# Performance work log

Hardware: AMD Instinct MI355X
Metric: run time of the kernel (lower is better)

The kernel has to match this reference:

```python
import jax, jax.numpy as jnp
import numpy as np

EPS = 1e-4
HEADS = 16
DH = 64


def setup_inputs() -> dict:
    key = jax.random.key(0)
    ks = jax.random.split(key, 5)
    b, t, d = 2, 2048, 1024
    return {
        "X": jax.random.normal(ks[0], (b, t, d), dtype=jnp.float32),
        "W_in": jax.random.normal(ks[1], (HEADS * 4 * DH, d), dtype=jnp.float32) * (1.0 / np.sqrt(d)),
        "b_in": jax.random.normal(ks[2], (HEADS * 4 * DH,), dtype=jnp.float32) * 0.01,
        "W_out": jax.random.normal(ks[3], (d, HEADS * DH), dtype=jnp.float32) * (1.0 / np.sqrt(HEADS * DH)),
        "b_out": jax.random.normal(ks[4], (d,), dtype=jnp.float32) * 0.01,
    }


def reference(X, W_in, b_in, W_out, b_out):
    b, t, d = X.shape
    # project_in: [b,t,h*4*dh] -> [b,t,h,4*dh] -> [b,h,t,4*dh]
    P = jnp.einsum('btd,ed->bte', X, W_in) + b_in
    P = P.reshape(b, t, HEADS, 4 * DH).transpose(0, 2, 1, 3)
    Q, K, V, G = jnp.split(P, 4, axis=-1)  # each [b,h,t,dh]
    # Euclidean cdist: sqrt(||q||^2 + ||k||^2 - 2 q.k), clamped at 0
    q2 = jnp.sum(Q * Q, axis=-1)[..., :, None]   # [b,h,t,1]
    k2 = jnp.sum(K * K, axis=-1)[..., None, :]   # [b,h,1,t]
    qk = jnp.einsum('bhqd,bhkd->bhqk', Q, K)
    dist = jnp.sqrt(jnp.maximum(q2 + k2 - 2.0 * qk, 0.0))
    # Shepard weights: (eps + dist)^-2, normalized over keys
    W = (EPS + dist) ** (-2)
    W = W / (EPS + jnp.sum(W, axis=-1, keepdims=True))
    A = jnp.einsum('bhqk,bhkd->bhqd', W, V)
    # gate, merge heads: [b,h,t,dh] -> [b,t,h*dh]
    H = (G * A).transpose(0, 2, 1, 3).reshape(b, t, HEADS * DH)
    Y = jnp.einsum('bte,de->btd', H, W_out) + b_out
    return Y
```

## Files before the change

### kernel.cpp

```cpp
#include <hip/hip_runtime.h>
#include <math.h>

#define EPS 1e-4f


typedef __attribute__((ext_vector_type(8))) short bf16x8;
typedef __attribute__((ext_vector_type(4))) float f32x4;

#define MFMA(a, b, c) __builtin_amdgcn_mfma_f32_16x16x32_bf16(a, b, c, 0, 0, 0)

__device__ __forceinline__ unsigned short f2b(float f) {
    unsigned int u = __float_as_uint(f);
    u += 0x7fffu + ((u >> 16) & 1u);
    return (unsigned short)(u >> 16);
}
__device__ __forceinline__ float b2f(unsigned short u) {
    return __uint_as_float(((unsigned int)u) << 16);
}
__device__ __forceinline__ unsigned int cvtpk(float a, float b) {
    unsigned int r;
    asm("v_cvt_pk_bf16_f32 %0, %1, %2" : "=v"(r) : "v"(a), "v"(b));
    return r;
}

__global__ __launch_bounds__(256)
void sga_f2b(const float* __restrict__ src, unsigned short* __restrict__ dst, int n8) {
    int i = blockIdx.x * 256 + threadIdx.x;
    const int stride = gridDim.x * 256;
    for (; i < n8; i += stride) {
        const float4* s = (const float4*)src + i * 2;
        float4 a = s[0], b = s[1];
        uint4 o;
        o.x = (unsigned)f2b(a.x) | ((unsigned)f2b(a.y) << 16);
        o.y = (unsigned)f2b(a.z) | ((unsigned)f2b(a.w) << 16);
        o.z = (unsigned)f2b(b.x) | ((unsigned)f2b(b.y) << 16);
        o.w = (unsigned)f2b(b.z) | ((unsigned)f2b(b.w) << 16);
        *((uint4*)dst + i) = o;
    }
}

__global__ __launch_bounds__(256)
void sga_gemm1(const unsigned short* __restrict__ Xb, const unsigned short* __restrict__ Wb,
               const float* __restrict__ bin,
               unsigned short* __restrict__ Qb, unsigned short* __restrict__ Kb,
               unsigned short* __restrict__ Vt, unsigned short* __restrict__ Gb)
{
    __shared__ unsigned short As[128 * 40];
    __shared__ unsigned short Bs[128 * 40];
    const int tid = threadIdx.x;
    const int lane = tid & 63, w = tid >> 6;
    const int lr = lane & 15, lg = lane >> 4;
    const int wm = w & 1, wn = w >> 1;
    const int m0 = blockIdx.y * 128, n0 = blockIdx.x * 128;
    const int r0 = tid >> 2, c0 = tid & 3;

    const unsigned short* Ap = Xb + (m0 + r0) * 1024 + c0 * 8;
    const unsigned short* Bp = Wb + (n0 + r0) * 1024 + c0 * 8;
    bf16x8 pa0 = *(const bf16x8*)Ap;
    bf16x8 pa1 = *(const bf16x8*)(Ap + 64 * 1024);
    bf16x8 pb0 = *(const bf16x8*)Bp;
    bf16x8 pb1 = *(const bf16x8*)(Bp + 64 * 1024);
    unsigned short* Aw = &As[r0 * 40 + c0 * 8];
    unsigned short* Bw = &Bs[r0 * 40 + c0 * 8];

    f32x4 acc[4][4] = {};

    for (int kt = 0; kt < 32; ++kt) {
        __syncthreads();
        *(bf16x8*)Aw = pa0; *(bf16x8*)(Aw + 64 * 40) = pa1;
        *(bf16x8*)Bw = pb0; *(bf16x8*)(Bw + 64 * 40) = pb1;
        __syncthreads();
        if (kt < 31) {
            Ap += 32; Bp += 32;
            pa0 = *(const bf16x8*)Ap; pa1 = *(const bf16x8*)(Ap + 64 * 1024);
            pb0 = *(const bf16x8*)Bp; pb1 = *(const bf16x8*)(Bp + 64 * 1024);
        }
        bf16x8 af[4], bfr[4];
        #pragma unroll
        for (int i = 0; i < 4; ++i)
            af[i] = *(const bf16x8*)&As[(wm * 64 + i * 16 + lr) * 40 + lg * 8];
        #pragma unroll
        for (int i = 0; i < 4; ++i)
            bfr[i] = *(const bf16x8*)&Bs[(wn * 64 + i * 16 + lr) * 40 + lg * 8];
        #pragma unroll
        for (int mi = 0; mi < 4; ++mi)
            #pragma unroll
            for (int ni = 0; ni < 4; ++ni)
                acc[mi][ni] = MFMA(af[mi], bfr[ni], acc[mi][ni]);
    }

    const int bb = m0 >> 11;
    #pragma unroll
    for (int mf = 0; mf < 4; ++mf) {
        const int tbase = m0 + wm * 64 + mf * 16 + lg * 4;
        const int tloc = tbase & 2047;
        #pragma unroll
        for (int nf = 0; nf < 4; ++nf) {
            const int n = n0 + wn * 64 + nf * 16 + lr;
            const int h = n >> 8, cc = n & 255;
            const int part = cc >> 6, j = cc & 63;
            const int bh = bb * 16 + h;
            const float bz = bin[n];
            f32x4 v = acc[mf][nf];
            unsigned short e0 = f2b(v[0] + bz), e1 = f2b(v[1] + bz),
                           e2 = f2b(v[2] + bz), e3 = f2b(v[3] + bz);
            if (part == 2) {
                ushort4 pk = make_ushort4(e0, e1, e2, e3);
                *(ushort4*)&Vt[(bh * 64 + j) * 2048 + tloc] = pk;
            } else {
                unsigned short* dst = (part == 0) ? Qb : ((part == 1) ? Kb : Gb);
                unsigned short vv[4] = {e0, e1, e2, e3};
                #pragma unroll
                for (int r = 0; r < 4; ++r)
                    dst[(bh * 2048 + tloc + r) * 64 + j] = vv[r];
            }
        }
    }
}

__global__ __launch_bounds__(256)
void sga_norms(const unsigned short* __restrict__ Qb, const unsigned short* __restrict__ Kb,
               float* __restrict__ q2s, float* __restrict__ k2s)
{
    const int idx = blockIdx.x * 256 + threadIdx.x;
    const unsigned short* q = Qb + idx * 64;
    const unsigned short* k = Kb + idx * 64;
    float sq = 0.f, sk = 0.f;
    #pragma unroll
    for (int c = 0; c < 8; ++c) {
        bf16x8 a = *(const bf16x8*)(q + c * 8);
        bf16x8 b = *(const bf16x8*)(k + c * 8);
        #pragma unroll
        for (int e = 0; e < 8; ++e) {
            float f = b2f((unsigned short)a[e]); sq += f * f;
            float g = b2f((unsigned short)b[e]); sk += g * g;
        }
    }
    q2s[idx] = sq;
    k2s[idx] = sk;
}

__global__ __launch_bounds__(256, 3)
void sga_attn(const unsigned short* __restrict__ Qb, const unsigned short* __restrict__ Kb,
              const unsigned short* __restrict__ Vt,
              const float* __restrict__ q2s, const float* __restrict__ k2s,
              unsigned short* __restrict__ Op0, unsigned short* __restrict__ Op1,
              unsigned short* __restrict__ Op2,
              float* __restrict__ Sw0, float* __restrict__ Sw1, float* __restrict__ Sw2)
{
    __shared__ unsigned short Klds[2 * 4096];
    __shared__ unsigned short Vlds[2 * 4096];
    __shared__ unsigned short Wlds[4 * 2048];

    const int tid = threadIdx.x;
    const int lane = tid & 63, w = tid >> 6;
    const int lr = lane & 15, lg = lane >> 4;

    const int qt = blockIdx.x, bh = blockIdx.y, half = blockIdx.z;
    const int q0 = qt * 128 + w * 32;
    const int kbeg = half * 11;
    const int kend = (half == 2) ? 32 : (kbeg + 11);

    unsigned short* wl = &Wlds[w * 2048];
    unsigned short* __restrict__ Op = (half == 0) ? Op0 : ((half == 1) ? Op1 : Op2);
    float* __restrict__ Sw = (half == 0) ? Sw0 : ((half == 1) ? Sw1 : Sw2);

    const int srow = w * 16 + (lane >> 2);
    const int sc = (lane & 3) * 2;
    const unsigned short* Kg = Kb + (bh * 2048 + srow) * 64 + sc * 8;
    const unsigned short* Vg = Vt + (bh * 64 + srow) * 2048 + sc * 8;
    const int swz0 = srow * 64 + ((sc ^ (srow & 7)) * 8);
    const int swz1 = srow * 64 + (((sc + 1) ^ (srow & 7)) * 8);

    bf16x8 qf[2][2];
    #pragma unroll
    for (int g = 0; g < 2; ++g) {
        const unsigned short* qp = Qb + (bh * 2048 + q0 + g * 16 + lr) * 64 + lg * 8;
        qf[g][0] = *(const bf16x8*)qp;
        qf[g][1] = *(const bf16x8*)(qp + 32);
    }
    float q2v[2];
    q2v[0] = q2s[bh * 2048 + q0 + lr];
    q2v[1] = q2s[bh * 2048 + q0 + 16 + lr];

    f32x4 oacc[2][4] = {};
    float sumw[2] = {0.f, 0.f};

    uint4 ks0, ks1, vs0, vs1;
    {
        const unsigned short* kp = Kg + kbeg * 4096;
        ks0 = *(const uint4*)kp; ks1 = *(const uint4*)(kp + 8);
        const unsigned short* vp = Vg + kbeg * 64;
        vs0 = *(const uint4*)vp; vs1 = *(const uint4*)(vp + 8);
    }
    *(uint4*)&Klds[swz0] = ks0; *(uint4*)&Klds[swz1] = ks1;
    *(uint4*)&Vlds[swz0] = vs0; *(uint4*)&Vlds[swz1] = vs1;
    __syncthreads();

    int buf = 0;
    for (int kt = kbeg; kt < kend; ++kt) {
        const int k0 = kt * 64;
        const bool more = (kt + 1 < kend);

        if (more) {
            const unsigned short* kp = Kg + (kt + 1) * 4096;
            ks0 = *(const uint4*)kp; ks1 = *(const uint4*)(kp + 8);
            const unsigned short* vp = Vg + (kt + 1) * 64;
            vs0 = *(const uint4*)vp; vs1 = *(const uint4*)(vp + 8);
        }

        f32x4 k2v[4];
        #pragma unroll
        for (int nf = 0; nf < 4; ++nf)
            k2v[nf] = *(const f32x4*)&k2s[bh * 2048 + k0 + nf * 16 + lg * 4];

        f32x4 sa[2][4] = {};
        const unsigned short* kb = &Klds[buf * 4096];
        __builtin_amdgcn_s_setprio(1);
        #pragma unroll
        for (int nf = 0; nf < 4; ++nf) {
            const int row = nf * 16 + lr;
            bf16x8 kf0 = *(const bf16x8*)&kb[row * 64 + ((lg ^ (row & 7)) * 8)];
            bf16x8 kf1 = *(const bf16x8*)&kb[row * 64 + (((4 + lg) ^ (row & 7)) * 8)];
            #pragma unroll
            for (int g = 0; g < 2; ++g) {
                sa[g][nf] = MFMA(kf0, qf[g][0], sa[g][nf]);
                sa[g][nf] = MFMA(kf1, qf[g][1], sa[g][nf]);
            }
        }
        __builtin_amdgcn_s_setprio(0);

        #pragma unroll
        for (int g = 0; g < 2; ++g) {
            const int row = g * 16 + lr;
            #pragma unroll
            for (int nf = 0; nf < 4; ++nf) {
                float wv[4];
                #pragma unroll
                for (int r = 0; r < 4; ++r) {
                    float d2 = fmaf(-2.0f, sa[g][nf][r], q2v[g] + k2v[nf][r]);
                    d2 = fmaxf(d2, 1e-8f);
                    wv[r] = __builtin_amdgcn_rcpf(d2);
                    sumw[g] += wv[r];
                }
                uint2 pk;
                pk.x = cvtpk(wv[0], wv[1]);
                pk.y = cvtpk(wv[2], wv[3]);
                const int c = 2 * nf + (lg >> 1);
                *(uint2*)&wl[row * 64 + ((c ^ (row & 7)) * 8) + (lg & 1) * 4] = pk;
            }
        }

        bf16x8 pa[2][2];
        #pragma unroll
        for (int g = 0; g < 2; ++g) {
            const int row = g * 16 + lr;
            pa[g][0] = *(const bf16x8*)&wl[row * 64 + ((lg ^ (row & 7)) * 8)];
            pa[g][1] = *(const bf16x8*)&wl[row * 64 + (((4 + lg) ^ (row & 7)) * 8)];
        }
        const unsigned short* vb = &Vlds[buf * 4096];
        __builtin_amdgcn_s_setprio(1);
        #pragma unroll
        for (int vf = 0; vf < 4; ++vf) {
            const int row = vf * 16 + lr;
            bf16x8 v0 = *(const bf16x8*)&vb[row * 64 + ((lg ^ (row & 7)) * 8)];
            bf16x8 v1 = *(const bf16x8*)&vb[row * 64 + (((4 + lg) ^ (row & 7)) * 8)];
            #pragma unroll
            for (int g = 0; g < 2; ++g) {
                oacc[g][vf] = MFMA(pa[g][0], v0, oacc[g][vf]);
                oacc[g][vf] = MFMA(pa[g][1], v1, oacc[g][vf]);
            }
        }
        __builtin_amdgcn_s_setprio(0);

        if (more) {
            const int bo = (buf ^ 1) * 4096;
            *(uint4*)&Klds[bo + swz0] = ks0; *(uint4*)&Klds[bo + swz1] = ks1;
            *(uint4*)&Vlds[bo + swz0] = vs0; *(uint4*)&Vlds[bo + swz1] = vs1;
            __syncthreads();
            buf ^= 1;
        }
    }

    #pragma unroll
    for (int g = 0; g < 2; ++g) {
        sumw[g] += __shfl_xor(sumw[g], 16, 64);
        sumw[g] += __shfl_xor(sumw[g], 32, 64);
    }

    #pragma unroll
    for (int g = 0; g < 2; ++g) {
        #pragma unroll
        for (int vf = 0; vf < 4; ++vf) {
            #pragma unroll
            for (int r = 0; r < 4; ++r) {
                const int t = q0 + g * 16 + lg * 4 + r;
                const int dh = vf * 16 + lr;
                Op[(bh * 2048 + t) * 64 + dh] = f2b(oacc[g][vf][r]);
            }
        }
    }
    if (lg == 0) {
        Sw[bh * 2048 + q0 + lr]      = sumw[0];
        Sw[bh * 2048 + q0 + 16 + lr] = sumw[1];
    }
}

__global__ __launch_bounds__(256)
void sga_combine(const unsigned short* __restrict__ Op0, const unsigned short* __restrict__ Op1,
                 const unsigned short* __restrict__ Op2,
                 const float* __restrict__ Sw0, const float* __restrict__ Sw1,
                 const float* __restrict__ Sw2,
                 const unsigned short* __restrict__ Gb, unsigned short* __restrict__ Hb)
{
    const int idx = blockIdx.x * 256 + threadIdx.x;
    const int t16 = idx >> 4;
    const int dq = (idx & 15) << 2;
    ushort4 a4 = *(const ushort4*)&Op0[t16 * 64 + dq];
    ushort4 b4 = *(const ushort4*)&Op1[t16 * 64 + dq];
    ushort4 c4 = *(const ushort4*)&Op2[t16 * 64 + dq];
    ushort4 g4 = *(const ushort4*)&Gb[t16 * 64 + dq];
    const float s = Sw0[t16] + Sw1[t16] + Sw2[t16];
    const float inv = __builtin_amdgcn_rcpf(EPS + s);
    const int bh = t16 >> 11, tloc = t16 & 2047;
    const int bb = bh >> 4, h = bh & 15;
    ushort4 o;
    o.x = f2b((b2f(a4.x) + b2f(b4.x) + b2f(c4.x)) * inv * b2f(g4.x));
    o.y = f2b((b2f(a4.y) + b2f(b4.y) + b2f(c4.y)) * inv * b2f(g4.y));
    o.z = f2b((b2f(a4.z) + b2f(b4.z) + b2f(c4.z)) * inv * b2f(g4.z));
    o.w = f2b((b2f(a4.w) + b2f(b4.w) + b2f(c4.w)) * inv * b2f(g4.w));
    *(ushort4*)&Hb[(bb * 2048 + tloc) * 1024 + h * 64 + dq] = o;
}

__global__ __launch_bounds__(256)
void sga_gemm2(const unsigned short* __restrict__ Hb, const unsigned short* __restrict__ Wb,
               const float* __restrict__ bout, float* __restrict__ Y)
{
    __shared__ unsigned short As[128 * 40];
    __shared__ unsigned short Bs[128 * 40];
    const int tid = threadIdx.x;
    const int lane = tid & 63, w = tid >> 6;
    const int lr = lane & 15, lg = lane >> 4;
    const int wm = w & 1, wn = w >> 1;
    const int m0 = blockIdx.y * 128, n0 = blockIdx.x * 128;
    const int r0 = tid >> 2, c0 = tid & 3;

    const unsigned short* Ap = Hb + (m0 + r0) * 1024 + c0 * 8;
    const unsigned short* Bp = Wb + (n0 + r0) * 1024 + c0 * 8;
    bf16x8 pa0 = *(const bf16x8*)Ap;
    bf16x8 pa1 = *(const bf16x8*)(Ap + 64 * 1024);
    bf16x8 pb0 = *(const bf16x8*)Bp;
    bf16x8 pb1 = *(const bf16x8*)(Bp + 64 * 1024);
    unsigned short* Aw = &As[r0 * 40 + c0 * 8];
    unsigned short* Bw = &Bs[r0 * 40 + c0 * 8];

    f32x4 acc[4][4] = {};

    for (int kt = 0; kt < 32; ++kt) {
        __syncthreads();
        *(bf16x8*)Aw = pa0; *(bf16x8*)(Aw + 64 * 40) = pa1;
        *(bf16x8*)Bw = pb0; *(bf16x8*)(Bw + 64 * 40) = pb1;
        __syncthreads();
        if (kt < 31) {
            Ap += 32; Bp += 32;
            pa0 = *(const bf16x8*)Ap; pa1 = *(const bf16x8*)(Ap + 64 * 1024);
            pb0 = *(const bf16x8*)Bp; pb1 = *(const bf16x8*)(Bp + 64 * 1024);
        }
        bf16x8 af[4], bfr[4];
        #pragma unroll
        for (int i = 0; i < 4; ++i)
            af[i] = *(const bf16x8*)&As[(wm * 64 + i * 16 + lr) * 40 + lg * 8];
        #pragma unroll
        for (int i = 0; i < 4; ++i)
            bfr[i] = *(const bf16x8*)&Bs[(wn * 64 + i * 16 + lr) * 40 + lg * 8];
        #pragma unroll
        for (int mi = 0; mi < 4; ++mi)
            #pragma unroll
            for (int ni = 0; ni < 4; ++ni)
                acc[mi][ni] = MFMA(af[mi], bfr[ni], acc[mi][ni]);
    }

    #pragma unroll
    for (int mf = 0; mf < 4; ++mf) {
        const int m = m0 + wm * 64 + mf * 16 + lg * 4;
        #pragma unroll
        for (int nf = 0; nf < 4; ++nf) {
            const int n = n0 + wn * 64 + nf * 16 + lr;
            const float bz = bout[n];
            f32x4 v = acc[mf][nf];
            #pragma unroll
            for (int r = 0; r < 4; ++r)
                Y[(m + r) * 1024 + n] = v[r] + bz;
        }
    }
}

extern "C" void kernel_launch(void* const* d_in, const int* in_sizes, int n_in,
                              void* d_out, int out_size, void* d_ws, size_t ws_size,
                              hipStream_t stream) {
    const float* X    = (const float*)d_in[0];
    const float* Win  = (const float*)d_in[1];
    const float* bin  = (const float*)d_in[2];
    const float* Wout = (const float*)d_in[3];
    const float* bout = (const float*)d_in[4];
    float* Y = (float*)d_out;

    const int PER = 32 * 2048 * 64;
    unsigned short* Qb   = (unsigned short*)d_ws;
    unsigned short* Kb   = Qb + PER;
    unsigned short* Vt   = Kb + PER;
    unsigned short* Gb   = Vt + PER;
    unsigned short* Hb   = Gb + PER;
    unsigned short* Xb   = Hb + PER;
    unsigned short* Winb = Xb + PER;
    unsigned short* Woutb= Winb + PER;
    float* q2s = (float*)(Woutb + 1024 * 1024);
    float* k2s = q2s + 32 * 2048;
    float* Sw0 = k2s + 32 * 2048;
    float* Sw1 = Sw0 + 32 * 2048;
    float* Sw2 = Sw1 + 32 * 2048;
    unsigned short* Op2 = (unsigned short*)(Sw2 + 32 * 2048);
    unsigned short* Op0 = Xb;
    unsigned short* Op1 = Winb;

    sga_f2b<<<1024, 256, 0, stream>>>(X, Xb, 524288);
    sga_f2b<<<1024, 256, 0, stream>>>(Win, Winb, 524288);
    sga_f2b<<<256, 256, 0, stream>>>(Wout, Woutb, 131072);
    sga_gemm1<<<dim3(32, 32), 256, 0, stream>>>(Xb, Winb, bin, Qb, Kb, Vt, Gb);
    sga_norms<<<256, 256, 0, stream>>>(Qb, Kb, q2s, k2s);
    sga_attn <<<dim3(16, 32, 3), 256, 0, stream>>>(Qb, Kb, Vt, q2s, k2s,
                                                   Op0, Op1, Op2, Sw0, Sw1, Sw2);
    sga_combine<<<4096, 256, 0, stream>>>(Op0, Op1, Op2, Sw0, Sw1, Sw2, Gb, Hb);
    sga_gemm2<<<dim3(8, 32), 256, 0, stream>>>(Hb, Woutb, bout, Y);
}
```

Baseline: 160.6 us.

## Use direct global-to-LDS loads with swizzle in GEMMs, fuse norms, widen combine

Both GEMMs now stage tiles through global_load_lds into XOR-swizzled 64-wide K tiles, which halves the number of K iterations and drops register staging. The prefetch overlap that the old register double-buffering gave is lost. The separate norms kernel is removed: squared norms of Q and K are computed in the gemm1 epilogue with wave shuffles, which saves a launch and a re-read of Q and K. The combine kernel processes 8 elements per thread, halving its grid.

```diff
diff --git a/kernel.cpp b/kernel.cpp
--- a/kernel.cpp
+++ b/kernel.cpp
@@ -5,6 +5,7 @@
 
 
 typedef __attribute__((ext_vector_type(8))) short bf16x8;
+typedef __attribute__((ext_vector_type(8))) unsigned short u16x8;
 typedef __attribute__((ext_vector_type(4))) float f32x4;
 
 #define MFMA(a, b, c) __builtin_amdgcn_mfma_f32_16x16x32_bf16(a, b, c, 0, 0, 0)
@@ -21,6 +22,12 @@
     unsigned int r;
     asm("v_cvt_pk_bf16_f32 %0, %1, %2" : "=v"(r) : "v"(a), "v"(b));
     return r;
+}
+
+typedef __attribute__((address_space(1))) const unsigned int as1_u32;
+typedef __attribute__((address_space(3))) unsigned int as3_u32;
+__device__ __forceinline__ void gl_lds16(const unsigned short* g, unsigned short* l) {
+    __builtin_amdgcn_global_load_lds((as1_u32*)g, (as3_u32*)l, 16, 0, 0);
 }
 
 __global__ __launch_bounds__(256)
@@ -43,57 +50,64 @@
 void sga_gemm1(const unsigned short* __restrict__ Xb, const unsigned short* __restrict__ Wb,
                const float* __restrict__ bin,
                unsigned short* __restrict__ Qb, unsigned short* __restrict__ Kb,
-               unsigned short* __restrict__ Vt, unsigned short* __restrict__ Gb)
+               unsigned short* __restrict__ Vt, unsigned short* __restrict__ Gb,
+               float* __restrict__ q2s, float* __restrict__ k2s)
 {
-    __shared__ unsigned short As[128 * 40];
-    __shared__ unsigned short Bs[128 * 40];
+    __shared__ unsigned short As[128 * 64];
+    __shared__ unsigned short Bs[128 * 64];
     const int tid = threadIdx.x;
     const int lane = tid & 63, w = tid >> 6;
     const int lr = lane & 15, lg = lane >> 4;
     const int wm = w & 1, wn = w >> 1;
     const int m0 = blockIdx.y * 128, n0 = blockIdx.x * 128;
-    const int r0 = tid >> 2, c0 = tid & 3;
-
-    const unsigned short* Ap = Xb + (m0 + r0) * 1024 + c0 * 8;
-    const unsigned short* Bp = Wb + (n0 + r0) * 1024 + c0 * 8;
-    bf16x8 pa0 = *(const bf16x8*)Ap;
-    bf16x8 pa1 = *(const bf16x8*)(Ap + 64 * 1024);
-    bf16x8 pb0 = *(const bf16x8*)Bp;
-    bf16x8 pb1 = *(const bf16x8*)(Bp + 64 * 1024);
-    unsigned short* Aw = &As[r0 * 40 + c0 * 8];
-    unsigned short* Bw = &Bs[r0 * 40 + c0 * 8];
+
+    const int sr = tid >> 3, sc8 = tid & 7;
+    const int gch = sc8 ^ (sr & 7);
+    const unsigned short* aBase = Xb + (m0 + sr) * 1024 + gch * 8;
+    const unsigned short* bBase = Wb + (n0 + sr) * 1024 + gch * 8;
+    unsigned short* aDst = &As[w * 512];
+    unsigned short* bDst = &Bs[w * 512];
 
     f32x4 acc[4][4] = {};
 
-    for (int kt = 0; kt < 32; ++kt) {
+    for (int kt = 0; kt < 16; ++kt) {
         __syncthreads();
-        *(bf16x8*)Aw = pa0; *(bf16x8*)(Aw + 64 * 40) = pa1;
-        *(bf16x8*)Bw = pb0; *(bf16x8*)(Bw + 64 * 40) = pb1;
+        #pragma unroll
+        for (int c = 0; c < 4; ++c)
+            gl_lds16(aBase + c * 32768 + kt * 64, aDst + c * 2048);
+        #pragma unroll
+        for (int c = 0; c < 4; ++c)
+            gl_lds16(bBase + c * 32768 + kt * 64, bDst + c * 2048);
         __syncthreads();
-        if (kt < 31) {
-            Ap += 32; Bp += 32;
-            pa0 = *(const bf16x8*)Ap; pa1 = *(const bf16x8*)(Ap + 64 * 1024);
-            pb0 = *(const bf16x8*)Bp; pb1 = *(const bf16x8*)(Bp + 64 * 1024);
-        }
-        bf16x8 af[4], bfr[4];
-        #pragma unroll
-        for (int i = 0; i < 4; ++i)
-            af[i] = *(const bf16x8*)&As[(wm * 64 + i * 16 + lr) * 40 + lg * 8];
-        #pragma unroll
-        for (int i = 0; i < 4; ++i)
-            bfr[i] = *(const bf16x8*)&Bs[(wn * 64 + i * 16 + lr) * 40 + lg * 8];
-        #pragma unroll
-        for (int mi = 0; mi < 4; ++mi)
-            #pragma unroll
-            for (int ni = 0; ni < 4; ++ni)
-                acc[mi][ni] = MFMA(af[mi], bfr[ni], acc[mi][ni]);
+
+        #pragma unroll
+        for (int ks = 0; ks < 2; ++ks) {
+            bf16x8 af[4], bfr[4];
+            #pragma unroll
+            for (int i = 0; i < 4; ++i) {
+                const int row = wm * 64 + i * 16 + lr;
+                af[i] = *(const bf16x8*)&As[row * 64 + (((ks * 4 + lg) ^ (row & 7)) * 8)];
+            }
+            #pragma unroll
+            for (int i = 0; i < 4; ++i) {
+                const int row = wn * 64 + i * 16 + lr;
+                bfr[i] = *(const bf16x8*)&Bs[row * 64 + (((ks * 4 + lg) ^ (row & 7)) * 8)];
+            }
+            #pragma unroll
+            for (int mi = 0; mi < 4; ++mi)
+                #pragma unroll
+                for (int ni = 0; ni < 4; ++ni)
+                    acc[mi][ni] = MFMA(af[mi], bfr[ni], acc[mi][ni]);
+        }
     }
 
     const int bb = m0 >> 11;
+    const bool qkBlock = ((n0 & 128) == 0);
     #pragma unroll
     for (int mf = 0; mf < 4; ++mf) {
         const int tbase = m0 + wm * 64 + mf * 16 + lg * 4;
         const int tloc = tbase & 2047;
+        float s2[4] = {0.f, 0.f, 0.f, 0.f};
         #pragma unroll
         for (int nf = 0; nf < 4; ++nf) {
             const int n = n0 + wn * 64 + nf * 16 + lr;
@@ -104,6 +118,11 @@
             f32x4 v = acc[mf][nf];
             unsigned short e0 = f2b(v[0] + bz), e1 = f2b(v[1] + bz),
                            e2 = f2b(v[2] + bz), e3 = f2b(v[3] + bz);
+            if (qkBlock) {
+                float f0 = b2f(e0), f1 = b2f(e1), f2 = b2f(e2), f3 = b2f(e3);
+                s2[0] += f0 * f0; s2[1] += f1 * f1;
+                s2[2] += f2 * f2; s2[3] += f3 * f3;
+            }
             if (part == 2) {
                 ushort4 pk = make_ushort4(e0, e1, e2, e3);
                 *(ushort4*)&Vt[(bh * 64 + j) * 2048 + tloc] = pk;
@@ -115,29 +134,18 @@
                     dst[(bh * 2048 + tloc + r) * 64 + j] = vv[r];
             }
         }
-    }
-}
-
-__global__ __launch_bounds__(256)
-void sga_norms(const unsigned short* __restrict__ Qb, const unsigned short* __restrict__ Kb,
-               float* __restrict__ q2s, float* __restrict__ k2s)
-{
-    const int idx = blockIdx.x * 256 + threadIdx.x;
-    const unsigned short* q = Qb + idx * 64;
-    const unsigned short* k = Kb + idx * 64;
-    float sq = 0.f, sk = 0.f;
-    #pragma unroll
-    for (int c = 0; c < 8; ++c) {
-        bf16x8 a = *(const bf16x8*)(q + c * 8);
-        bf16x8 b = *(const bf16x8*)(k + c * 8);
-        #pragma unroll
-        for (int e = 0; e < 8; ++e) {
-            float f = b2f((unsigned short)a[e]); sq += f * f;
-            float g = b2f((unsigned short)b[e]); sk += g * g;
-        }
-    }
-    q2s[idx] = sq;
-    k2s[idx] = sk;
+        if (qkBlock) {
+            const int bh = bb * 16 + (n0 >> 8);
+            float* __restrict__ dstn = wn ? k2s : q2s;
+            #pragma unroll
+            for (int r = 0; r < 4; ++r) {
+                float v = s2[r];
+                v += __shfl_xor(v, 1, 64); v += __shfl_xor(v, 2, 64);
+                v += __shfl_xor(v, 4, 64); v += __shfl_xor(v, 8, 64);
+                if (lr == 0) dstn[bh * 2048 + ((tloc + r) & 2047)] = v;
+            }
+        }
+    }
 }
 
 __global__ __launch_bounds__(256, 3)
@@ -314,70 +322,73 @@
                  const unsigned short* __restrict__ Gb, unsigned short* __restrict__ Hb)
 {
     const int idx = blockIdx.x * 256 + threadIdx.x;
-    const int t16 = idx >> 4;
-    const int dq = (idx & 15) << 2;
-    ushort4 a4 = *(const ushort4*)&Op0[t16 * 64 + dq];
-    ushort4 b4 = *(const ushort4*)&Op1[t16 * 64 + dq];
-    ushort4 c4 = *(const ushort4*)&Op2[t16 * 64 + dq];
-    ushort4 g4 = *(const ushort4*)&Gb[t16 * 64 + dq];
+    const int t16 = idx >> 3;
+    const int dq = (idx & 7) << 3;
+    u16x8 a = *(const u16x8*)&Op0[t16 * 64 + dq];
+    u16x8 b = *(const u16x8*)&Op1[t16 * 64 + dq];
+    u16x8 c = *(const u16x8*)&Op2[t16 * 64 + dq];
+    u16x8 g = *(const u16x8*)&Gb[t16 * 64 + dq];
     const float s = Sw0[t16] + Sw1[t16] + Sw2[t16];
     const float inv = __builtin_amdgcn_rcpf(EPS + s);
     const int bh = t16 >> 11, tloc = t16 & 2047;
     const int bb = bh >> 4, h = bh & 15;
-    ushort4 o;
-    o.x = f2b((b2f(a4.x) + b2f(b4.x) + b2f(c4.x)) * inv * b2f(g4.x));
-    o.y = f2b((b2f(a4.y) + b2f(b4.y) + b2f(c4.y)) * inv * b2f(g4.y));
-    o.z = f2b((b2f(a4.z) + b2f(b4.z) + b2f(c4.z)) * inv * b2f(g4.z));
-    o.w = f2b((b2f(a4.w) + b2f(b4.w) + b2f(c4.w)) * inv * b2f(g4.w));
-    *(ushort4*)&Hb[(bb * 2048 + tloc) * 1024 + h * 64 + dq] = o;
+    u16x8 o;
+    #pragma unroll
+    for (int j = 0; j < 8; ++j)
+        o[j] = f2b((b2f(a[j]) + b2f(b[j]) + b2f(c[j])) * inv * b2f(g[j]));
+    *(u16x8*)&Hb[(bb * 2048 + tloc) * 1024 + h * 64 + dq] = o;
 }
 
 __global__ __launch_bounds__(256)
 void sga_gemm2(const unsigned short* __restrict__ Hb, const unsigned short* __restrict__ Wb,
                const float* __restrict__ bout, float* __restrict__ Y)
 {
-    __shared__ unsigned short As[128 * 40];
-    __shared__ unsigned short Bs[128 * 40];
+    __shared__ unsigned short As[128 * 64];
+    __shared__ unsigned short Bs[128 * 64];
     const int tid = threadIdx.x;
     const int lane = tid & 63, w = tid >> 6;
     const int lr = lane & 15, lg = lane >> 4;
     const int wm = w & 1, wn = w >> 1;
     const int m0 = blockIdx.y * 128, n0 = blockIdx.x * 128;
-    const int r0 = tid >> 2, c0 = tid & 3;
-
-    const unsigned short* Ap = Hb + (m0 + r0) * 1024 + c0 * 8;
-    const unsigned short* Bp = Wb + (n0 + r0) * 1024 + c0 * 8;
-    bf16x8 pa0 = *(const bf16x8*)Ap;
-    bf16x8 pa1 = *(const bf16x8*)(Ap + 64 * 1024);
-    bf16x8 pb0 = *(const bf16x8*)Bp;
-    bf16x8 pb1 = *(const bf16x8*)(Bp + 64 * 1024);
-    unsigned short* Aw = &As[r0 * 40 + c0 * 8];
-    unsigned short* Bw = &Bs[r0 * 40 + c0 * 8];
+
+    const int sr = tid >> 3, sc8 = tid & 7;
+    const int gch = sc8 ^ (sr & 7);
+    const unsigned short* aBase = Hb + (m0 + sr) * 1024 + gch * 8;
+    const unsigned short* bBase = Wb + (n0 + sr) * 1024 + gch * 8;
+    unsigned short* aDst = &As[w * 512];
+    unsigned short* bDst = &Bs[w * 512];
 
     f32x4 acc[4][4] = {};
 
-    for (int kt = 0; kt < 32; ++kt) {
+    for (int kt = 0; kt < 16; ++kt) {
         __syncthreads();
-        *(bf16x8*)Aw = pa0; *(bf16x8*)(Aw + 64 * 40) = pa1;
-        *(bf16x8*)Bw = pb0; *(bf16x8*)(Bw + 64 * 40) = pb1;
+        #pragma unroll
+        for (int c = 0; c < 4; ++c)
+            gl_lds16(aBase + c * 32768 + kt * 64, aDst + c * 2048);
+        #pragma unroll
+        for (int c = 0; c < 4; ++c)
+            gl_lds16(bBase + c * 32768 + kt * 64, bDst + c * 2048);
         __syncthreads();
-        if (kt < 31) {
-            Ap += 32; Bp += 32;
-            pa0 = *(const bf16x8*)Ap; pa1 = *(const bf16x8*)(Ap + 64 * 1024);
-            pb0 = *(const bf16x8*)Bp; pb1 = *(const bf16x8*)(Bp + 64 * 1024);
-        }
-        bf16x8 af[4], bfr[4];
-        #pragma unroll
-        for (int i = 0; i < 4; ++i)
-            af[i] = *(const bf16x8*)&As[(wm * 64 + i * 16 + lr) * 40 + lg * 8];
-        #pragma unroll
-        for (int i = 0; i < 4; ++i)
-            bfr[i] = *(const bf16x8*)&Bs[(wn * 64 + i * 16 + lr) * 40 + lg * 8];
-        #pragma unroll
-        for (int mi = 0; mi < 4; ++mi)
-            #pragma unroll
-            for (int ni = 0; ni < 4; ++ni)
-                acc[mi][ni] = MFMA(af[mi], bfr[ni], acc[mi][ni]);
+
+        #pragma unroll
+        for (int ks = 0; ks < 2; ++ks) {
+            bf16x8 af[4], bfr[4];
+            #pragma unroll
+            for (int i = 0; i < 4; ++i) {
+                const int row = wm * 64 + i * 16 + lr;
+                af[i] = *(const bf16x8*)&As[row * 64 + (((ks * 4 + lg) ^ (row & 7)) * 8)];
+            }
+            #pragma unroll
+            for (int i = 0; i < 4; ++i) {
+                const int row = wn * 64 + i * 16 + lr;
+                bfr[i] = *(const bf16x8*)&Bs[row * 64 + (((ks * 4 + lg) ^ (row & 7)) * 8)];
+            }
+            #pragma unroll
+            for (int mi = 0; mi < 4; ++mi)
+                #pragma unroll
+                for (int ni = 0; ni < 4; ++ni)
+                    acc[mi][ni] = MFMA(af[mi], bfr[ni], acc[mi][ni]);
+        }
     }
 
     #pragma unroll
@@ -426,10 +437,9 @@
     sga_f2b<<<1024, 256, 0, stream>>>(X, Xb, 524288);
     sga_f2b<<<1024, 256, 0, stream>>>(Win, Winb, 524288);
     sga_f2b<<<256, 256, 0, stream>>>(Wout, Woutb, 131072);
-    sga_gemm1<<<dim3(32, 32), 256, 0, stream>>>(Xb, Winb, bin, Qb, Kb, Vt, Gb);
-    sga_norms<<<256, 256, 0, stream>>>(Qb, Kb, q2s, k2s);
+    sga_gemm1<<<dim3(32, 32), 256, 0, stream>>>(Xb, Winb, bin, Qb, Kb, Vt, Gb, q2s, k2s);
     sga_attn <<<dim3(16, 32, 3), 256, 0, stream>>>(Qb, Kb, Vt, q2s, k2s,
                                                    Op0, Op1, Op2, Sw0, Sw1, Sw2);
-    sga_combine<<<4096, 256, 0, stream>>>(Op0, Op1, Op2, Sw0, Sw1, Sw2, Gb, Hb);
+    sga_combine<<<2048, 256, 0, stream>>>(Op0, Op1, Op2, Sw0, Sw1, Sw2, Gb, Hb);
     sga_gemm2<<<dim3(8, 32), 256, 0, stream>>>(Hb, Woutb, bout, Y);
 }
```

New measurement: 153.1 us. -4.7%, faster.
